# Kernel tuning notes

Hardware: AMD Instinct MI355X
Metric: run time of the kernel (lower is better)

## Reference

```python
import jax, jax.numpy as jnp
import numpy as np
from jax import lax

# Config matching init_kwargs
STRIDE = 1
PAD = 1


def setup_inputs() -> dict:
    key = jax.random.key(0)
    k1, k2, k3, k4 = jax.random.split(key, 4)
    x = jax.random.normal(k1, (8, 64, 128, 128), jnp.float32)
    # offset conv: out_channels = 2*kh*kw = 18, no bias; small init so offsets are moderate
    w_offset = jax.random.normal(k2, (18, 64, 3, 3), jnp.float32) * 0.01
    w_deform = jax.random.normal(k3, (64, 64, 3, 3), jnp.float32) * 0.05
    b_deform = jax.random.normal(k4, (64,), jnp.float32) * 0.05
    return {"x": x, "w_offset": w_offset, "w_deform": w_deform, "b_deform": b_deform}


def _deform_conv2d(x, offset, weight, bias, stride, pad):
    """torchvision.ops.deform_conv2d (v1, offset_groups=1) in pure jax.

    x: [B,C,H,W], offset: [B,2*kh*kw,Ho,Wo] ordered (dy,dx) per kernel tap,
    weight: [O,C,kh,kw], bias: [O].
    """
    B, C, H, W = x.shape
    O, _, kh, kw = weight.shape
    Ho, Wo = offset.shape[2], offset.shape[3]
    K = kh * kw

    off = offset.reshape(B, K, 2, Ho, Wo)  # [...,0]=dy, [...,1]=dx
    ky, kx = jnp.meshgrid(jnp.arange(kh), jnp.arange(kw), indexing="ij")
    base_y = (jnp.arange(Ho) * stride - pad).astype(x.dtype)  # [Ho]
    base_x = (jnp.arange(Wo) * stride - pad).astype(x.dtype)  # [Wo]
    # sampling positions [B,K,Ho,Wo]
    py = base_y[None, None, :, None] + ky.reshape(1, K, 1, 1).astype(x.dtype) + off[:, :, 0]
    px = base_x[None, None, None, :] + kx.reshape(1, K, 1, 1).astype(x.dtype) + off[:, :, 1]

    y0f = jnp.floor(py)
    x0f = jnp.floor(px)
    wy = py - y0f  # bilinear fractional weights [B,K,Ho,Wo]
    wx = px - x0f
    y0 = y0f.astype(jnp.int32)
    x0 = x0f.astype(jnp.int32)

    def gather(yi, xi):
        # zero-padded gather: out-of-bounds samples contribute 0
        valid = (yi >= 0) & (yi < H) & (xi >= 0) & (xi < W)
        yc = jnp.clip(yi, 0, H - 1)
        xc = jnp.clip(xi, 0, W - 1)
        # per-batch fancy gather -> [B, C, K, Ho, Wo]
        g = jax.vmap(lambda im, yy, xx: im[:, yy, xx])(x, yc, xc)
        return g * valid[:, None].astype(x.dtype)

    one = jnp.asarray(1, x.dtype)
    val = (gather(y0, x0) * ((one - wy) * (one - wx))[:, None]
           + gather(y0, x0 + 1) * ((one - wy) * wx)[:, None]
           + gather(y0 + 1, x0) * (wy * (one - wx))[:, None]
           + gather(y0 + 1, x0 + 1) * (wy * wx)[:, None])  # [B,C,K,Ho,Wo]

    out = jnp.einsum("ock,bckij->boij", weight.reshape(O, C, K), val)
    return out + bias[None, :, None, None]


def reference(x, w_offset, w_deform, b_deform):
    # offset-predicting conv (no bias)
    offset = lax.conv_general_dilated(
        x, w_offset, window_strides=(STRIDE, STRIDE),
        padding=[(PAD, PAD), (PAD, PAD)],
        dimension_numbers=("NCHW", "OIHW", "NCHW"))
    return _deform_conv2d(x, offset, w_deform, b_deform, STRIDE, PAD)
```

## Files before the change

### kernel.cpp

```cpp
#include <hip/hip_runtime.h>

#define BATCH 8
#define CIN 64
#define H 128
#define W 128
#define OCH 64
#define HW (H*W)
#define OFFCH 18

using f16x8 = __attribute__((ext_vector_type(8))) _Float16;
using f32x4 = __attribute__((ext_vector_type(4))) float;

static __device__ __forceinline__ int iclamp(int v, int lo, int hi) {
    return v < lo ? lo : (v > hi ? hi : v);
}
static __device__ __forceinline__ f16x8 splat8(_Float16 v) {
    return (f16x8){v, v, v, v, v, v, v, v};
}
static __device__ __forceinline__ unsigned packh2(float a, float b) {
    union { _Float16 h[2]; unsigned u; } pk;
    pk.h[0] = (_Float16)a; pk.h[1] = (_Float16)b;
    return pk.u;
}

__global__ __launch_bounds__(256) void transpose_x_kernel(
    const float* __restrict__ x, _Float16* __restrict__ xt)
{
    __shared__ float ls[CIN][129];
    int bid = blockIdx.x;
    int b = bid >> 7, y = bid & 127;
    int t = threadIdx.x;

    const float* xb = x + (size_t)b * CIN * HW + (size_t)y * W;
    #pragma unroll 4
    for (int i = 0; i < 32; ++i) {
        int c = i * 2 + (t >> 7);
        ls[c][t & 127] = xb[(size_t)c * HW + (t & 127)];
    }
    __syncthreads();

    _Float16* xo = xt + (size_t)(b * H + y) * W * CIN;
    #pragma unroll 4
    for (int i = 0; i < 16; ++i) {
        int px = i * 8 + (t >> 5);
        int c  = (t & 31) * 2;
        _Float16 a0 = (_Float16)ls[c][px];
        _Float16 a1 = (_Float16)ls[c + 1][px];
        union { _Float16 h[2]; unsigned int u; } pk;
        pk.h[0] = a0; pk.h[1] = a1;
        *(unsigned int*)&xo[(size_t)px * CIN + c] = pk.u;
    }
}

__global__ __launch_bounds__(256) void prep_wdf_kernel(
    const float* __restrict__ w, _Float16* __restrict__ wdf)
{
    int i = blockIdx.x * 256 + threadIdx.x;
    if (i >= 9 * 2 * 4 * 64 * 8) return;
    int j    = i & 7;
    int lane = (i >> 3) & 63;
    int mt   = (i >> 9) & 3;
    int cs   = (i >> 11) & 1;
    int tap  = i >> 12;
    int oc = mt * 16 + (lane & 15);
    int c  = cs * 32 + (lane >> 4) * 8 + j;
    wdf[i] = (_Float16)w[(oc * CIN + c) * 9 + tap];
}

__global__ __launch_bounds__(256) void prep_wof_kernel(
    const float* __restrict__ w, _Float16* __restrict__ wof)
{
    int i = blockIdx.x * 256 + threadIdx.x;
    if (i >= 9 * 2 * 2 * 64 * 8) return;
    int j    = i & 7;
    int lane = (i >> 3) & 63;
    int mt   = (i >> 9) & 1;
    int cs   = (i >> 10) & 1;
    int tap  = i >> 11;
    int oc = mt * 16 + (lane & 15);
    int c  = cs * 32 + (lane >> 4) * 8 + j;
    wof[i] = (oc < OFFCH) ? (_Float16)w[(oc * CIN + c) * 9 + tap] : (_Float16)0.f;
}

__global__ __launch_bounds__(512, 2) void fused_deform_kernel(
    const _Float16* __restrict__ xt, const f16x8* __restrict__ wof,
    const f16x8* __restrict__ wdf, const float* __restrict__ bias,
    float* __restrict__ out)
{
    __shared__ _Float16 band[6 * 128 * CIN];
    __shared__ uint4 recs[2 * 128 * 9];
    __shared__ unsigned int offs_f[2 * 128 * 9];

    int bid  = blockIdx.x;
    int b    = bid & 7;
    int y    = (bid >> 3) * 2;
    int tid  = threadIdx.x;
    int lane = tid & 63;
    int wave = tid >> 6;
    int l15  = lane & 15;
    int lk   = lane >> 4;
    int rw   = wave >> 2;
    int yo   = y + rw;
    int pxbase = (wave & 3) * 32;
    int p0   = pxbase + l15;
    int p1   = p0 + 16;

    int ylo = y - 2 < 0 ? 0 : y - 2;
    int yhi = y + 3 > H - 1 ? H - 1 : y + 3;
    int nrm1 = yhi - ylo;

    const _Float16* xb = xt + (size_t)b * HW * CIN;

    {
        #pragma unroll
        for (int r = 0; r < 6; ++r) {
            int gy = ylo + r;
            if (gy > yhi) break;
            #pragma unroll
            for (int i = 0; i < 2; ++i) {
                int linear = i * 512 + tid;
                int spx = linear >> 3;
                int sjl = linear & 7;
                int sjp = sjl ^ (spx & 7);
                *(f16x8*)&band[(((size_t)r * 128 + spx) * 8 + sjp) * 8] =
                    *(const f16x8*)&xb[((size_t)gy * W + spx) * CIN + sjl * 8];
            }
        }
    }
    __syncthreads();

    f32x4 oacc[2][2];
    #pragma unroll
    for (int mt = 0; mt < 2; ++mt)
        #pragma unroll
        for (int nt = 0; nt < 2; ++nt) oacc[mt][nt] = (f32x4){0.f, 0.f, 0.f, 0.f};

    #pragma unroll
    for (int tap = 0; tap < 9; ++tap) {
        int ky = tap / 3, kx = tap - 3 * ky;
        int yy = yo - 1 + ky;
        bool iny = (yy >= 0 && yy < H);
        int ry = yy - ylo;
        int pos0 = p0 - 1 + kx;
        int pos1 = p1 - 1 + kx;
        #pragma unroll
        for (int cs = 0; cs < 2; ++cs) {
            const f16x8* wf = wof + (size_t)((tap * 2 + cs) * 2) * 64 + lane;
            f16x8 a0 = wf[0];
            f16x8 a1 = wf[64];
            f16x8 b0 = splat8((_Float16)0.f), b1 = splat8((_Float16)0.f);
            if (iny && pos0 >= 0 && pos0 < W) {
                int jp = (cs * 4 + lk) ^ (pos0 & 7);
                b0 = *(const f16x8*)&band[(((size_t)ry * 128 + pos0) * 8 + jp) * 8];
            }
            if (iny && pos1 >= 0 && pos1 < W) {
                int jp = (cs * 4 + lk) ^ (pos1 & 7);
                b1 = *(const f16x8*)&band[(((size_t)ry * 128 + pos1) * 8 + jp) * 8];
            }
            oacc[0][0] = __builtin_amdgcn_mfma_f32_16x16x32_f16(a0, b0, oacc[0][0], 0, 0, 0);
            oacc[1][0] = __builtin_amdgcn_mfma_f32_16x16x32_f16(a1, b0, oacc[1][0], 0, 0, 0);
            oacc[0][1] = __builtin_amdgcn_mfma_f32_16x16x32_f16(a0, b1, oacc[0][1], 0, 0, 0);
            oacc[1][1] = __builtin_amdgcn_mfma_f32_16x16x32_f16(a1, b1, oacc[1][1], 0, 0, 0);
        }
    }

    int rbase0 = (rw * 128 + p0) * 9;
    int rbase1 = (rw * 128 + p1) * 9;
    auto build = [&](int tap, float offy, float offx, int p, int rbase) {
        int ky = tap / 3, kx = tap - 3 * ky;
        float py  = (float)(yo - 1 + ky) + offy;
        float pxf = (float)(p  - 1 + kx) + offx;
        float y0f = floorf(py), x0f = floorf(pxf);
        float fy = py - y0f, fx = pxf - x0f;
        int y0 = (int)y0f, x0 = (int)x0f;
        int y1 = y0 + 1, x1 = x0 + 1;
        float m00 = (1.f - fy) * (1.f - fx);
        float m01 = (1.f - fy) * fx;
        float m10 = fy * (1.f - fx);
        float m11 = fy * fx;
        if (y0 < 0 || y0 >= H) { m00 = 0.f; m01 = 0.f; }
        if (y1 < 0 || y1 >= H) { m10 = 0.f; m11 = 0.f; }
        if (x0 < 0 || x0 >= W) { m00 = 0.f; m10 = 0.f; }
        if (x1 < 0 || x1 >= W) { m01 = 0.f; m11 = 0.f; }
        int y0c = iclamp(y0, 0, H - 1), y1c = iclamp(y1, 0, H - 1);
        int x0c = iclamp(x0, 0, W - 1), x1c = iclamp(x1, 0, W - 1);
        int ry0 = y0c - ylo, ry1 = y1c - ylo;
        unsigned o0 = (ry0 < 0 || ry0 > nrm1) ? 0x8000u : 0u;
        unsigned o1 = (ry1 < 0 || ry1 > nrm1) ? 0x8000u : 0u;
        int r0 = iclamp(ry0, 0, 5), r1 = iclamp(ry1, 0, 5);
        unsigned f0 = (unsigned)(((r0 * 128 + x0c) << 3) | (x0c & 7)) | o0;
        unsigned f1 = (unsigned)(((r0 * 128 + x1c) << 3) | (x1c & 7)) | o0;
        unsigned f2 = (unsigned)(((r1 * 128 + x0c) << 3) | (x0c & 7)) | o1;
        unsigned f3 = (unsigned)(((r1 * 128 + x1c) << 3) | (x1c & 7)) | o1;
        uint4 rc;
        rc.x = packh2(m00, m01);
        rc.y = packh2(m10, m11);
        rc.z = f0 | (f1 << 16);
        rc.w = f2 | (f3 << 16);
        recs[rbase + tap] = rc;
        offs_f[rbase + tap] = packh2(offy, offx);
    };
    build(2 * lk,     oacc[0][0][0], oacc[0][0][1], p0, rbase0);
    build(2 * lk + 1, oacc[0][0][2], oacc[0][0][3], p0, rbase0);
    build(2 * lk,     oacc[0][1][0], oacc[0][1][1], p1, rbase1);
    build(2 * lk + 1, oacc[0][1][2], oacc[0][1][3], p1, rbase1);
    if (lk == 0) {
        build(8, oacc[1][0][0], oacc[1][0][1], p0, rbase0);
        build(8, oacc[1][1][0], oacc[1][1][1], p1, rbase1);
    }

    f32x4 acc[4][2];
    #pragma unroll
    for (int mt = 0; mt < 4; ++mt)
        #pragma unroll
        for (int nt = 0; nt < 2; ++nt) acc[mt][nt] = (f32x4){0.f, 0.f, 0.f, 0.f};

    const char* bb = (const char*)band;

    #pragma unroll
    for (int tap = 0; tap < 9; ++tap) {
        f16x8 bfr[2][2];
        #pragma unroll
        for (int nt = 0; nt < 2; ++nt) {
            int rbase = nt ? rbase1 : rbase0;
            int pp    = nt ? p1 : p0;
            uint4 rc = recs[rbase + tap];
            union { unsigned u; _Float16 h[2]; } mA, mB;
            mA.u = rc.x; mB.u = rc.y;
            _Float16 h00 = mA.h[0], h01 = mA.h[1], h10 = mB.h[0], h11 = mB.h[1];
            int f0 = rc.z & 0xffff, f1 = rc.z >> 16;
            int f2 = rc.w & 0xffff, f3 = rc.w >> 16;
            bool fall = ((rc.z | rc.w) & 0x8000u) != 0;
            int a00 = (((f0 >> 3) & 1023) << 7) + ((lk ^ (f0 & 7)) << 4);
            int a01 = (((f1 >> 3) & 1023) << 7) + ((lk ^ (f1 & 7)) << 4);
            int a10 = (((f2 >> 3) & 1023) << 7) + ((lk ^ (f2 & 7)) << 4);
            int a11 = (((f3 >> 3) & 1023) << 7) + ((lk ^ (f3 & 7)) << 4);

            f16x8 g00 = *(const f16x8*)(bb + a00);
            f16x8 g01 = *(const f16x8*)(bb + a01);
            f16x8 g10 = *(const f16x8*)(bb + a10);
            f16x8 g11 = *(const f16x8*)(bb + a11);
            bfr[0][nt] = g00 * splat8(h00) + g01 * splat8(h01)
                       + g10 * splat8(h10) + g11 * splat8(h11);
            f16x8 k00 = *(const f16x8*)(bb + (a00 ^ 64));
            f16x8 k01 = *(const f16x8*)(bb + (a01 ^ 64));
            f16x8 k10 = *(const f16x8*)(bb + (a10 ^ 64));
            f16x8 k11 = *(const f16x8*)(bb + (a11 ^ 64));
            bfr[1][nt] = k00 * splat8(h00) + k01 * splat8(h01)
                       + k10 * splat8(h10) + k11 * splat8(h11);

            if (fall) {
                union { unsigned u; _Float16 h[2]; } of;
                of.u = offs_f[rbase + tap];
                float offy = (float)of.h[0], offx = (float)of.h[1];
                int ky = tap / 3, kx = tap - 3 * ky;
                float py  = (float)(yo - 1 + ky) + offy;
                float pxf = (float)(pp - 1 + kx) + offx;
                float y0f = floorf(py), x0f = floorf(pxf);
                float fy = py - y0f, fx = pxf - x0f;
                int y0 = (int)y0f, x0 = (int)x0f;
                int y1 = y0 + 1, x1 = x0 + 1;
                float n00 = (1.f - fy) * (1.f - fx);
                float n01 = (1.f - fy) * fx;
                float n10 = fy * (1.f - fx);
                float n11 = fy * fx;
                if (y0 < 0 || y0 >= H) { n00 = 0.f; n01 = 0.f; }
                if (y1 < 0 || y1 >= H) { n10 = 0.f; n11 = 0.f; }
                if (x0 < 0 || x0 >= W) { n00 = 0.f; n10 = 0.f; }
                if (x1 < 0 || x1 >= W) { n01 = 0.f; n11 = 0.f; }
                int y0c = iclamp(y0, 0, H - 1), y1c = iclamp(y1, 0, H - 1);
                int x0c = iclamp(x0, 0, W - 1), x1c = iclamp(x1, 0, W - 1);
                _Float16 q00 = (_Float16)n00, q01 = (_Float16)n01;
                _Float16 q10 = (_Float16)n10, q11 = (_Float16)n11;
                size_t i00 = ((size_t)y0c * W + x0c) * CIN, i01 = ((size_t)y0c * W + x1c) * CIN;
                size_t i10 = ((size_t)y1c * W + x0c) * CIN, i11 = ((size_t)y1c * W + x1c) * CIN;
                int c0 = lk * 8;
                bfr[0][nt] = (*(const f16x8*)&xb[i00 + c0]) * splat8(q00)
                           + (*(const f16x8*)&xb[i01 + c0]) * splat8(q01)
                           + (*(const f16x8*)&xb[i10 + c0]) * splat8(q10)
                           + (*(const f16x8*)&xb[i11 + c0]) * splat8(q11);
                int c1 = 32 + lk * 8;
                bfr[1][nt] = (*(const f16x8*)&xb[i00 + c1]) * splat8(q00)
                           + (*(const f16x8*)&xb[i01 + c1]) * splat8(q01)
                           + (*(const f16x8*)&xb[i10 + c1]) * splat8(q10)
                           + (*(const f16x8*)&xb[i11 + c1]) * splat8(q11);
            }
        }

        #pragma unroll
        for (int cs = 0; cs < 2; ++cs) {
            const f16x8* wf = wdf + (size_t)((tap * 2 + cs) * 4) * 64 + lane;
            #pragma unroll
            for (int mt = 0; mt < 4; ++mt) {
                f16x8 af = wf[mt * 64];
                acc[mt][0] = __builtin_amdgcn_mfma_f32_16x16x32_f16(af, bfr[cs][0], acc[mt][0], 0, 0, 0);
                acc[mt][1] = __builtin_amdgcn_mfma_f32_16x16x32_f16(af, bfr[cs][1], acc[mt][1], 0, 0, 0);
            }
        }
    }

    #pragma unroll
    for (int mt = 0; mt < 4; ++mt) {
        #pragma unroll
        for (int nt = 0; nt < 2; ++nt) {
            int pp = nt ? p1 : p0;
            #pragma unroll
            for (int r = 0; r < 4; ++r) {
                int oc = mt * 16 + lk * 4 + r;
                out[((size_t)b * OCH + oc) * HW + (size_t)yo * W + pp] = acc[mt][nt][r] + bias[oc];
            }
        }
    }
}

extern "C" void kernel_launch(void* const* d_in, const int* in_sizes, int n_in,
                              void* d_out, int out_size, void* d_ws, size_t ws_size,
                              hipStream_t stream) {
    const float* x     = (const float*)d_in[0];
    const float* w_off = (const float*)d_in[1];
    const float* w_def = (const float*)d_in[2];
    const float* b_def = (const float*)d_in[3];
    float* out = (float*)d_out;

    _Float16* xt  = (_Float16*)d_ws;
    _Float16* wdf = xt + (size_t)BATCH * HW * CIN;
    _Float16* wof = wdf + 36864;

    transpose_x_kernel<<<BATCH * H, 256, 0, stream>>>(x, xt);
    prep_wdf_kernel<<<(36864 + 255) / 256, 256, 0, stream>>>(w_def, wdf);
    prep_wof_kernel<<<(18432 + 255) / 256, 256, 0, stream>>>(w_off, wof);
    fused_deform_kernel<<<BATCH * H / 2, 512, 0, stream>>>(
        xt, (const f16x8*)wof, (const f16x8*)wdf, b_def, out);
}
```

Measured before the change: 55.12 us.

## Process four output rows per block and pass sampling records via wave shuffles

```diff
diff --git a/kernel.cpp b/kernel.cpp
--- a/kernel.cpp
+++ b/kernel.cpp
@@ -82,49 +82,42 @@
     wof[i] = (oc < OFFCH) ? (_Float16)w[(oc * CIN + c) * 9 + tap] : (_Float16)0.f;
 }
 
-__global__ __launch_bounds__(512, 2) void fused_deform_kernel(
+__global__ __launch_bounds__(1024, 4) void fused_deform_kernel(
     const _Float16* __restrict__ xt, const f16x8* __restrict__ wof,
     const f16x8* __restrict__ wdf, const float* __restrict__ bias,
     float* __restrict__ out)
 {
-    __shared__ _Float16 band[6 * 128 * CIN];
-    __shared__ uint4 recs[2 * 128 * 9];
-    __shared__ unsigned int offs_f[2 * 128 * 9];
+    __shared__ _Float16 band[8 * 128 * CIN];
 
     int bid  = blockIdx.x;
     int b    = bid & 7;
-    int y    = (bid >> 3) * 2;
+    int y    = (bid >> 3) * 4;
     int tid  = threadIdx.x;
     int lane = tid & 63;
     int wave = tid >> 6;
     int l15  = lane & 15;
     int lk   = lane >> 4;
-    int rw   = wave >> 2;
-    int yo   = y + rw;
+    int yo   = y + (wave >> 2);
     int pxbase = (wave & 3) * 32;
     int p0   = pxbase + l15;
     int p1   = p0 + 16;
 
     int ylo = y - 2 < 0 ? 0 : y - 2;
-    int yhi = y + 3 > H - 1 ? H - 1 : y + 3;
+    int yhi = y + 5 > H - 1 ? H - 1 : y + 5;
     int nrm1 = yhi - ylo;
 
     const _Float16* xb = xt + (size_t)b * HW * CIN;
 
     {
-        #pragma unroll
-        for (int r = 0; r < 6; ++r) {
+        int spx = tid >> 3;
+        int sjl = tid & 7;
+        int sjp = sjl ^ (spx & 7);
+        #pragma unroll
+        for (int r = 0; r < 8; ++r) {
             int gy = ylo + r;
             if (gy > yhi) break;
-            #pragma unroll
-            for (int i = 0; i < 2; ++i) {
-                int linear = i * 512 + tid;
-                int spx = linear >> 3;
-                int sjl = linear & 7;
-                int sjp = sjl ^ (spx & 7);
-                *(f16x8*)&band[(((size_t)r * 128 + spx) * 8 + sjp) * 8] =
-                    *(const f16x8*)&xb[((size_t)gy * W + spx) * CIN + sjl * 8];
-            }
+            *(f16x8*)&band[(((size_t)r * 128 + spx) * 8 + sjp) * 8] =
+                *(const f16x8*)&xb[((size_t)gy * W + spx) * CIN + sjl * 8];
         }
     }
     __syncthreads();
@@ -164,9 +157,11 @@
         }
     }
 
-    int rbase0 = (rw * 128 + p0) * 9;
-    int rbase1 = (rw * 128 + p1) * 9;
-    auto build = [&](int tap, float offy, float offx, int p, int rbase) {
+    uint4 rcA, rcB, rcC, rcD;
+    uint4 rc8a = {0,0,0,0}, rc8b = {0,0,0,0};
+    unsigned ofA, ofB, ofC, ofD, of8a = 0, of8b = 0;
+
+    auto build = [&](int tap, float offy, float offx, int p, uint4& rc, unsigned& of) {
         int ky = tap / 3, kx = tap - 3 * ky;
         float py  = (float)(yo - 1 + ky) + offy;
         float pxf = (float)(p  - 1 + kx) + offx;
@@ -187,26 +182,24 @@
         int ry0 = y0c - ylo, ry1 = y1c - ylo;
         unsigned o0 = (ry0 < 0 || ry0 > nrm1) ? 0x8000u : 0u;
         unsigned o1 = (ry1 < 0 || ry1 > nrm1) ? 0x8000u : 0u;
-        int r0 = iclamp(ry0, 0, 5), r1 = iclamp(ry1, 0, 5);
+        int r0 = iclamp(ry0, 0, 7), r1 = iclamp(ry1, 0, 7);
         unsigned f0 = (unsigned)(((r0 * 128 + x0c) << 3) | (x0c & 7)) | o0;
         unsigned f1 = (unsigned)(((r0 * 128 + x1c) << 3) | (x1c & 7)) | o0;
         unsigned f2 = (unsigned)(((r1 * 128 + x0c) << 3) | (x0c & 7)) | o1;
         unsigned f3 = (unsigned)(((r1 * 128 + x1c) << 3) | (x1c & 7)) | o1;
-        uint4 rc;
         rc.x = packh2(m00, m01);
         rc.y = packh2(m10, m11);
         rc.z = f0 | (f1 << 16);
         rc.w = f2 | (f3 << 16);
-        recs[rbase + tap] = rc;
-        offs_f[rbase + tap] = packh2(offy, offx);
+        of   = packh2(offy, offx);
     };
-    build(2 * lk,     oacc[0][0][0], oacc[0][0][1], p0, rbase0);
-    build(2 * lk + 1, oacc[0][0][2], oacc[0][0][3], p0, rbase0);
-    build(2 * lk,     oacc[0][1][0], oacc[0][1][1], p1, rbase1);
-    build(2 * lk + 1, oacc[0][1][2], oacc[0][1][3], p1, rbase1);
+    build(2 * lk,     oacc[0][0][0], oacc[0][0][1], p0, rcA, ofA);
+    build(2 * lk + 1, oacc[0][0][2], oacc[0][0][3], p0, rcB, ofB);
+    build(2 * lk,     oacc[0][1][0], oacc[0][1][1], p1, rcC, ofC);
+    build(2 * lk + 1, oacc[0][1][2], oacc[0][1][3], p1, rcD, ofD);
     if (lk == 0) {
-        build(8, oacc[1][0][0], oacc[1][0][1], p0, rbase0);
-        build(8, oacc[1][1][0], oacc[1][1][1], p1, rbase1);
+        build(8, oacc[1][0][0], oacc[1][0][1], p0, rc8a, of8a);
+        build(8, oacc[1][1][0], oacc[1][1][1], p1, rc8b, of8b);
     }
 
     f32x4 acc[4][2];
@@ -219,12 +212,23 @@
 
     #pragma unroll
     for (int tap = 0; tap < 9; ++tap) {
+        int src = (tap < 8) ? ((tap >> 1) * 16 + l15) : l15;
         f16x8 bfr[2][2];
         #pragma unroll
         for (int nt = 0; nt < 2; ++nt) {
-            int rbase = nt ? rbase1 : rbase0;
-            int pp    = nt ? p1 : p0;
-            uint4 rc = recs[rbase + tap];
+            int pp = nt ? p1 : p0;
+            uint4 rsel;
+            unsigned osel;
+            if (tap < 8) {
+                if (tap & 1) { rsel = nt ? rcD : rcB; osel = nt ? ofD : ofB; }
+                else         { rsel = nt ? rcC : rcA; osel = nt ? ofC : ofA; }
+            } else         { rsel = nt ? rc8b : rc8a; osel = nt ? of8b : of8a; }
+            uint4 rc;
+            rc.x = (unsigned)__shfl((int)rsel.x, src, 64);
+            rc.y = (unsigned)__shfl((int)rsel.y, src, 64);
+            rc.z = (unsigned)__shfl((int)rsel.z, src, 64);
+            rc.w = (unsigned)__shfl((int)rsel.w, src, 64);
+
             union { unsigned u; _Float16 h[2]; } mA, mB;
             mA.u = rc.x; mB.u = rc.y;
             _Float16 h00 = mA.h[0], h01 = mA.h[1], h10 = mB.h[0], h11 = mB.h[1];
@@ -249,41 +253,44 @@
             bfr[1][nt] = k00 * splat8(h00) + k01 * splat8(h01)
                        + k10 * splat8(h10) + k11 * splat8(h11);
 
-            if (fall) {
-                union { unsigned u; _Float16 h[2]; } of;
-                of.u = offs_f[rbase + tap];
-                float offy = (float)of.h[0], offx = (float)of.h[1];
-                int ky = tap / 3, kx = tap - 3 * ky;
-                float py  = (float)(yo - 1 + ky) + offy;
-                float pxf = (float)(pp - 1 + kx) + offx;
-                float y0f = floorf(py), x0f = floorf(pxf);
-                float fy = py - y0f, fx = pxf - x0f;
-                int y0 = (int)y0f, x0 = (int)x0f;
-                int y1 = y0 + 1, x1 = x0 + 1;
-                float n00 = (1.f - fy) * (1.f - fx);
-                float n01 = (1.f - fy) * fx;
-                float n10 = fy * (1.f - fx);
-                float n11 = fy * fx;
-                if (y0 < 0 || y0 >= H) { n00 = 0.f; n01 = 0.f; }
-                if (y1 < 0 || y1 >= H) { n10 = 0.f; n11 = 0.f; }
-                if (x0 < 0 || x0 >= W) { n00 = 0.f; n10 = 0.f; }
-                if (x1 < 0 || x1 >= W) { n01 = 0.f; n11 = 0.f; }
-                int y0c = iclamp(y0, 0, H - 1), y1c = iclamp(y1, 0, H - 1);
-                int x0c = iclamp(x0, 0, W - 1), x1c = iclamp(x1, 0, W - 1);
-                _Float16 q00 = (_Float16)n00, q01 = (_Float16)n01;
-                _Float16 q10 = (_Float16)n10, q11 = (_Float16)n11;
-                size_t i00 = ((size_t)y0c * W + x0c) * CIN, i01 = ((size_t)y0c * W + x1c) * CIN;
-                size_t i10 = ((size_t)y1c * W + x0c) * CIN, i11 = ((size_t)y1c * W + x1c) * CIN;
-                int c0 = lk * 8;
-                bfr[0][nt] = (*(const f16x8*)&xb[i00 + c0]) * splat8(q00)
-                           + (*(const f16x8*)&xb[i01 + c0]) * splat8(q01)
-                           + (*(const f16x8*)&xb[i10 + c0]) * splat8(q10)
-                           + (*(const f16x8*)&xb[i11 + c0]) * splat8(q11);
-                int c1 = 32 + lk * 8;
-                bfr[1][nt] = (*(const f16x8*)&xb[i00 + c1]) * splat8(q00)
-                           + (*(const f16x8*)&xb[i01 + c1]) * splat8(q01)
-                           + (*(const f16x8*)&xb[i10 + c1]) * splat8(q10)
-                           + (*(const f16x8*)&xb[i11 + c1]) * splat8(q11);
+            if (__any(fall)) {
+                unsigned ofu = (unsigned)__shfl((int)osel, src, 64);
+                if (fall) {
+                    union { unsigned u; _Float16 h[2]; } of;
+                    of.u = ofu;
+                    float offy = (float)of.h[0], offx = (float)of.h[1];
+                    int ky = tap / 3, kx = tap - 3 * ky;
+                    float py  = (float)(yo - 1 + ky) + offy;
+                    float pxf = (float)(pp - 1 + kx) + offx;
+                    float y0f = floorf(py), x0f = floorf(pxf);
+                    float fy = py - y0f, fx = pxf - x0f;
+                    int y0 = (int)y0f, x0 = (int)x0f;
+                    int y1 = y0 + 1, x1 = x0 + 1;
+                    float n00 = (1.f - fy) * (1.f - fx);
+                    float n01 = (1.f - fy) * fx;
+                    float n10 = fy * (1.f - fx);
+                    float n11 = fy * fx;
+                    if (y0 < 0 || y0 >= H) { n00 = 0.f; n01 = 0.f; }
+                    if (y1 < 0 || y1 >= H) { n10 = 0.f; n11 = 0.f; }
+                    if (x0 < 0 || x0 >= W) { n00 = 0.f; n10 = 0.f; }
+                    if (x1 < 0 || x1 >= W) { n01 = 0.f; n11 = 0.f; }
+                    int y0c = iclamp(y0, 0, H - 1), y1c = iclamp(y1, 0, H - 1);
+                    int x0c = iclamp(x0, 0, W - 1), x1c = iclamp(x1, 0, W - 1);
+                    _Float16 q00 = (_Float16)n00, q01 = (_Float16)n01;
+                    _Float16 q10 = (_Float16)n10, q11 = (_Float16)n11;
+                    size_t i00 = ((size_t)y0c * W + x0c) * CIN, i01 = ((size_t)y0c * W + x1c) * CIN;
+                    size_t i10 = ((size_t)y1c * W + x0c) * CIN, i11 = ((size_t)y1c * W + x1c) * CIN;
+                    int c0 = lk * 8;
+                    bfr[0][nt] = (*(const f16x8*)&xb[i00 + c0]) * splat8(q00)
+                               + (*(const f16x8*)&xb[i01 + c0]) * splat8(q01)
+                               + (*(const f16x8*)&xb[i10 + c0]) * splat8(q10)
+                               + (*(const f16x8*)&xb[i11 + c0]) * splat8(q11);
+                    int c1 = 32 + lk * 8;
+                    bfr[1][nt] = (*(const f16x8*)&xb[i00 + c1]) * splat8(q00)
+                               + (*(const f16x8*)&xb[i01 + c1]) * splat8(q01)
+                               + (*(const f16x8*)&xb[i10 + c1]) * splat8(q10)
+                               + (*(const f16x8*)&xb[i11 + c1]) * splat8(q11);
+                }
             }
         }
 
@@ -329,6 +336,6 @@
     transpose_x_kernel<<<BATCH * H, 256, 0, stream>>>(x, xt);
     prep_wdf_kernel<<<(36864 + 255) / 256, 256, 0, stream>>>(w_def, wdf);
     prep_wof_kernel<<<(18432 + 255) / 256, 256, 0, stream>>>(w_off, wof);
-    fused_deform_kernel<<<BATCH * H / 2, 512, 0, stream>>>(
+    fused_deform_kernel<<<BATCH * H / 4, 1024, 0, stream>>>(
         xt, (const f16x8*)wof, (const f16x8*)wdf, b_def, out);
 }
```

New measurement: 54.05 us. About the same (-1.9%).
